# Kernel tuning notes

Measured on AMD Instinct MI355X. Metric: run time of the kernel, lower is better.

Reference implementation:

```python
import jax, jax.numpy as jnp
import numpy as np

K = 3  # polynomial filter order

def gfgcn_layer(X, S, W, h, b):
    # X: [N, in], W: [in, out], h: [K], b: [out]
    X = X @ W
    X_out = h[0] * X
    Sx = X
    for k in range(1, K):
        Sx = S @ Sx                 # graph shift propagation
        X_out = X_out + h[k] * Sx   # scalar-weighted accumulate
    return X_out + b[None, :]


def setup_inputs() -> dict:
    key = jax.random.key(0)
    ks = jax.random.split(key, 12)
    N, in_dim, hid_dim, out_dim = 8192, 512, 128, 64
    # scale S so repeated propagation stays numerically tame
    S = jax.random.normal(ks[0], (N, N), dtype=jnp.float32) / jnp.sqrt(jnp.float32(N))
    X = jax.random.normal(ks[1], (N, in_dim), dtype=jnp.float32)
    def kaiming(k, shape):
        bound = np.sqrt(6.0 / shape[0])
        return jax.random.uniform(k, shape, jnp.float32, -bound, bound)
    W1 = kaiming(ks[2], (in_dim, hid_dim))
    W2 = kaiming(ks[3], (hid_dim, hid_dim))
    W3 = kaiming(ks[4], (hid_dim, out_dim))
    h1 = jnp.ones((K,), jnp.float32)
    h2 = jnp.ones((K,), jnp.float32)
    h3 = jnp.ones((K,), jnp.float32)
    b1 = jnp.zeros((hid_dim,), jnp.float32)
    b2 = jnp.zeros((hid_dim,), jnp.float32)
    b3 = jnp.zeros((out_dim,), jnp.float32)
    return {"S": S, "X": X, "W1": W1, "h1": h1, "b1": b1,
            "W2": W2, "h2": h2, "b2": b2, "W3": W3, "h3": h3, "b3": b3}


def reference(S, X, W1, h1, b1, W2, h2, b2, W3, h3, b3):
    # layer 1 + ReLU (dropout p=0 -> identity, batch_norm=False)
    X = jax.nn.relu(gfgcn_layer(X, S, W1, h1, b1))
    # layer 2 + ReLU
    X = jax.nn.relu(gfgcn_layer(X, S, W2, h2, b2))
    # last layer, last_act = Identity
    return gfgcn_layer(X, S, W3, h3, b3)
```

## Files before the change

kernel.cpp:

```cpp
#include <hip/hip_runtime.h>


typedef __attribute__((ext_vector_type(4))) float  f32x4;
typedef __attribute__((ext_vector_type(8))) __bf16 bf16x8;
typedef __attribute__((ext_vector_type(4))) __bf16 bf16x4;

__device__ __forceinline__ void gload_lds16(const __bf16* g, __bf16* l) {
    __builtin_amdgcn_global_load_lds(
        (const __attribute__((address_space(1))) void*)g,
        (__attribute__((address_space(3))) void*)l, 16, 0, 0);
}

__global__ void cvt_f32_bf16(const float4* __restrict__ in,
                             bf16x4* __restrict__ out, int n4) {
    int i  = blockIdx.x * blockDim.x + threadIdx.x;
    int st = gridDim.x * blockDim.x;
    for (; i < n4; i += st) {
        float4 v = in[i];
        bf16x4 o;
        o[0] = (__bf16)v.x; o[1] = (__bf16)v.y;
        o[2] = (__bf16)v.z; o[3] = (__bf16)v.w;
        out[i] = o;
    }
}

__global__ void cvt_transpose(const float* __restrict__ W,
                              __bf16* __restrict__ Wt, int Kd, int Md) {
    int i = blockIdx.x * blockDim.x + threadIdx.x;
    if (i < Kd * Md) {
        int k = i / Md, m = i % Md;
        Wt[(size_t)m * Kd + k] = (__bf16)W[i];
    }
}

template<int MF, int NF, int OUTMODE>
__global__ __launch_bounds__(256)
void gemm_rd(const __bf16* __restrict__ A, const __bf16* __restrict__ Bt,
             void* __restrict__ out, int K, int Kchunk, int Mtot, int Ntot)
{
    const int lane = threadIdx.x & 63;
    const int w    = threadIdx.x >> 6;
    const int l15  = lane & 15;
    const int quad = lane >> 4;

    const int m_base = blockIdx.x * (64 * MF) + w * (16 * MF);
    const int n_base = blockIdx.y * (16 * NF);
    const int kstart = blockIdx.z * Kchunk;

    const __bf16* Ap[MF];
    #pragma unroll
    for (int mf = 0; mf < MF; mf++)
        Ap[mf] = A + (size_t)(m_base + mf * 16 + l15) * K + kstart + quad * 8;
    const __bf16* Bp[NF];
    #pragma unroll
    for (int nf = 0; nf < NF; nf++)
        Bp[nf] = Bt + (size_t)(n_base + nf * 16 + l15) * K + kstart + quad * 8;

    f32x4 acc[MF][NF];
    #pragma unroll
    for (int mf = 0; mf < MF; mf++)
        #pragma unroll
        for (int nf = 0; nf < NF; nf++)
            acc[mf][nf] = (f32x4){0.f, 0.f, 0.f, 0.f};

    #pragma unroll 2
    for (int ks = 0; ks < Kchunk; ks += 32) {
        bf16x8 a[MF], b[NF];
        #pragma unroll
        for (int mf = 0; mf < MF; mf++) a[mf] = *(const bf16x8*)(Ap[mf] + ks);
        #pragma unroll
        for (int nf = 0; nf < NF; nf++) b[nf] = *(const bf16x8*)(Bp[nf] + ks);
        #pragma unroll
        for (int mf = 0; mf < MF; mf++)
            #pragma unroll
            for (int nf = 0; nf < NF; nf++)
                acc[mf][nf] = __builtin_amdgcn_mfma_f32_16x16x32_bf16(
                    a[mf], b[nf], acc[mf][nf], 0, 0, 0);
    }

    if (OUTMODE == 0) {
        float* P = (float*)out + (size_t)blockIdx.z * Mtot * Ntot;
        #pragma unroll
        for (int mf = 0; mf < MF; mf++) {
            const int rowb = m_base + mf * 16 + quad * 4;
            #pragma unroll
            for (int nf = 0; nf < NF; nf++) {
                const int col = n_base + nf * 16 + l15;
                *(f32x4*)(P + (size_t)col * Mtot + rowb) = acc[mf][nf];
            }
        }
    } else {
        __bf16* O = (__bf16*)out;
        #pragma unroll
        for (int mf = 0; mf < MF; mf++) {
            const int rowb = m_base + mf * 16 + quad * 4;
            #pragma unroll
            for (int nf = 0; nf < NF; nf++) {
                const int col = n_base + nf * 16 + l15;
                #pragma unroll
                for (int r = 0; r < 4; r++)
                    O[(size_t)(rowb + r) * Ntot + col] = (__bf16)acc[mf][nf][r];
            }
        }
    }
}

template<int NFW>
__global__ __launch_bounds__(256)
void sgemm_lds(const __bf16* __restrict__ A, const __bf16* __restrict__ Bt,
               float* __restrict__ P, int K, int Kchunk, int Mtot)
{
    constexpr int BN = 32 * NFW;
    __shared__ __bf16 Asm[2][64 * 32];
    __shared__ __bf16 Bsm[2][BN * 32];

    const int t    = threadIdx.x;
    const int lane = t & 63;
    const int w    = t >> 6;
    const int wm   = w >> 1;
    const int wn   = w & 1;
    const int l15  = lane & 15;
    const int quad = lane >> 4;

    const int m_block = blockIdx.x * 64;
    const int kstart  = blockIdx.z * Kchunk;

    const int rt  = t >> 2;
    const int qs  = (t & 3) ^ ((rt >> 1) & 3);
    const __bf16* gA  = A  + (size_t)(m_block + rt) * K + kstart + qs * 8;
    const __bf16* gB0 = Bt + (size_t)rt * K        + kstart + qs * 8;
    const __bf16* gB1 = Bt + (size_t)(64 + rt) * K + kstart + qs * 8;

    f32x4 acc[2][NFW];
    #pragma unroll
    for (int mf = 0; mf < 2; mf++)
        #pragma unroll
        for (int nf = 0; nf < NFW; nf++)
            acc[mf][nf] = (f32x4){0.f, 0.f, 0.f, 0.f};

    auto stage = [&](int buf, int ks) {
        gload_lds16(gA  + ks, &Asm[buf][t * 8]);
        gload_lds16(gB0 + ks, &Bsm[buf][t * 8]);
        if (NFW == 4)
            gload_lds16(gB1 + ks, &Bsm[buf][2048 + t * 8]);
    };

    int aoff[2], boff[NFW];
    #pragma unroll
    for (int mf = 0; mf < 2; mf++) {
        const int ar = wm * 32 + mf * 16 + l15;
        aoff[mf] = ar * 32 + (quad ^ ((ar >> 1) & 3)) * 8;
    }
    #pragma unroll
    for (int nf = 0; nf < NFW; nf++) {
        const int br = wn * 16 * NFW + nf * 16 + l15;
        boff[nf] = br * 32 + (quad ^ ((br >> 1) & 3)) * 8;
    }

    stage(0, 0);
    __syncthreads();

    int buf = 0;
    for (int ks = 0; ; ) {
        const int nks = ks + 32;
        if (nks < Kchunk) stage(buf ^ 1, nks);

        bf16x8 a[2], b[NFW];
        #pragma unroll
        for (int mf = 0; mf < 2; mf++)
            a[mf] = *(const bf16x8*)&Asm[buf][aoff[mf]];
        #pragma unroll
        for (int nf = 0; nf < NFW; nf++)
            b[nf] = *(const bf16x8*)&Bsm[buf][boff[nf]];

        #pragma unroll
        for (int mf = 0; mf < 2; mf++)
            #pragma unroll
            for (int nf = 0; nf < NFW; nf++)
                acc[mf][nf] = __builtin_amdgcn_mfma_f32_16x16x32_bf16(
                    a[mf], b[nf], acc[mf][nf], 0, 0, 0);

        ks = nks;
        if (ks >= Kchunk) break;
        __syncthreads();
        buf ^= 1;
    }

    float* Pz = P + (size_t)blockIdx.z * Mtot * BN;
    #pragma unroll
    for (int mf = 0; mf < 2; mf++) {
        const int rowb = m_block + wm * 32 + mf * 16 + quad * 4;
        #pragma unroll
        for (int nf = 0; nf < NFW; nf++) {
            const int col = wn * 16 * NFW + nf * 16 + l15;
            *(f32x4*)(Pz + (size_t)col * Mtot + rowb) = acc[mf][nf];
        }
    }
}

__global__ void reduce_partials(const float* __restrict__ P,
                                __bf16* __restrict__ Y, int total4,
                                int SP, int MN) {
    int i = blockIdx.x * blockDim.x + threadIdx.x;
    if (i >= total4) return;
    size_t base = (size_t)i * 4;
    float4 s = *(const float4*)(P + base);
    for (int sp = 1; sp < SP; sp++) {
        float4 v = *(const float4*)(P + (size_t)sp * MN + base);
        s.x += v.x; s.y += v.y; s.z += v.z; s.w += v.w;
    }
    bf16x4 o; o[0] = (__bf16)s.x; o[1] = (__bf16)s.y;
    o[2] = (__bf16)s.z; o[3] = (__bf16)s.w;
    *(bf16x4*)(Y + base) = o;
}

template<int RELU, int F32OUT>
__global__ void combine_out(const float* __restrict__ P,
                            const __bf16* __restrict__ Y0t,
                            const __bf16* __restrict__ Y1t,
                            const float* __restrict__ h,
                            const float* __restrict__ bias,
                            void* __restrict__ outp,
                            int F, int SP) {
    const int i = blockIdx.x * blockDim.x + threadIdx.x;
    const int total = F * 2048;
    if (i >= total) return;
    const int f  = i >> 11;
    const int n4 = i & 2047;
    const size_t base = (size_t)f * 8192 + (size_t)n4 * 4;
    const int MN = F * 8192;

    float4 s = *(const float4*)(P + base);
    for (int sp = 1; sp < SP; sp++) {
        float4 v = *(const float4*)(P + (size_t)sp * MN + base);
        s.x += v.x; s.y += v.y; s.z += v.z; s.w += v.w;
    }
    bf16x4 y0 = *(const bf16x4*)(Y0t + base);
    bf16x4 y1 = *(const bf16x4*)(Y1t + base);
    const float h0 = h[0], h1 = h[1], h2 = h[2], bb = bias[f];

    float v[4] = {s.x, s.y, s.z, s.w};
    #pragma unroll
    for (int r = 0; r < 4; r++) {
        float x = h0 * (float)y0[r] + h1 * (float)y1[r] + h2 * v[r] + bb;
        if (RELU) x = fmaxf(x, 0.0f);
        v[r] = x;
    }
    const int node = n4 * 4;
    if (F32OUT) {
        float* O = (float*)outp;
        #pragma unroll
        for (int r = 0; r < 4; r++) O[(size_t)(node + r) * F + f] = v[r];
    } else {
        __bf16* O = (__bf16*)outp;
        #pragma unroll
        for (int r = 0; r < 4; r++) O[(size_t)(node + r) * F + f] = (__bf16)v[r];
    }
}

extern "C" void kernel_launch(void* const* d_in, const int* in_sizes, int n_in,
                              void* d_out, int out_size, void* d_ws, size_t ws_size,
                              hipStream_t stream) {
    const float* S  = (const float*)d_in[0];
    const float* X  = (const float*)d_in[1];
    const float* W1 = (const float*)d_in[2];
    const float* h1 = (const float*)d_in[3];
    const float* b1 = (const float*)d_in[4];
    const float* W2 = (const float*)d_in[5];
    const float* h2 = (const float*)d_in[6];
    const float* b2 = (const float*)d_in[7];
    const float* W3 = (const float*)d_in[8];
    const float* h3 = (const float*)d_in[9];
    const float* b3 = (const float*)d_in[10];
    float* out = (float*)d_out;

    const int Nn = 8192, IN = 512, HID = 128, OUT = 64;

    char* ws = (char*)d_ws;
    size_t off = 0;
    auto carve = [&](size_t bytes) -> void* {
        void* p = ws + off;
        off += (bytes + 255) & ~(size_t)255;
        return p;
    };
    __bf16* Sb  = (__bf16*)carve((size_t)Nn * Nn  * 2);
    __bf16* Xb  = (__bf16*)carve((size_t)Nn * IN  * 2);
    __bf16* W1t = (__bf16*)carve((size_t)IN  * HID * 2);
    __bf16* W2t = (__bf16*)carve((size_t)HID * HID * 2);
    __bf16* W3t = (__bf16*)carve((size_t)HID * OUT * 2);
    __bf16* Y0t = (__bf16*)carve((size_t)HID * Nn * 2);
    __bf16* Y1t = (__bf16*)carve((size_t)HID * Nn * 2);
    __bf16* Act = (__bf16*)carve((size_t)Nn * HID * 2);
    size_t  base = off;

    const size_t per_split = (size_t)HID * Nn * 4;
    int SP = 1;
    while (SP < 8 && base + (size_t)(SP * 2) * per_split <= ws_size) SP *= 2;
    float* P = (float*)carve((size_t)SP * per_split);
    const int KCH = Nn / SP;

    {
        int n4 = Nn * Nn / 4;
        cvt_f32_bf16<<<dim3((n4 + 255) / 256), dim3(256), 0, stream>>>(
            (const float4*)S, (bf16x4*)Sb, n4);
        n4 = Nn * IN / 4;
        cvt_f32_bf16<<<dim3((n4 + 255) / 256), dim3(256), 0, stream>>>(
            (const float4*)X, (bf16x4*)Xb, n4);
    }
    cvt_transpose<<<dim3((IN * HID + 255) / 256), dim3(256), 0, stream>>>(W1, W1t, IN, HID);
    cvt_transpose<<<dim3((HID * HID + 255) / 256), dim3(256), 0, stream>>>(W2, W2t, HID, HID);
    cvt_transpose<<<dim3((HID * OUT + 255) / 256), dim3(256), 0, stream>>>(W3, W3t, HID, OUT);

    auto sgemm = [&](const __bf16* Bt, int F) {
        if (F == 128)
            sgemm_lds<4><<<dim3(Nn / 64, 1, SP), dim3(256), 0, stream>>>(
                Sb, Bt, P, Nn, KCH, Nn);
        else
            sgemm_lds<2><<<dim3(Nn / 64, 1, SP), dim3(256), 0, stream>>>(
                Sb, Bt, P, Nn, KCH, Nn);
    };
    auto reduceY = [&](__bf16* Y, int F) {
        int t4 = F * 2048;
        reduce_partials<<<dim3((t4 + 255) / 256), dim3(256), 0, stream>>>(
            P, Y, t4, SP, F * Nn);
    };

    gemm_rd<2, 4, 1><<<dim3(1, Nn / 64, 1), dim3(256), 0, stream>>>(
        W1t, Xb, Y0t, IN, IN, HID, Nn);
    sgemm(Y0t, HID);
    reduceY(Y1t, HID);
    sgemm(Y1t, HID);
    combine_out<1, 0><<<dim3(HID * 2048 / 256), dim3(256), 0, stream>>>(
        P, Y0t, Y1t, h1, b1, Act, HID, SP);

    gemm_rd<2, 4, 1><<<dim3(1, Nn / 64, 1), dim3(256), 0, stream>>>(
        W2t, Act, Y0t, HID, HID, HID, Nn);
    sgemm(Y0t, HID);
    reduceY(Y1t, HID);
    sgemm(Y1t, HID);
    combine_out<1, 0><<<dim3(HID * 2048 / 256), dim3(256), 0, stream>>>(
        P, Y0t, Y1t, h2, b2, Act, HID, SP);

    gemm_rd<1, 4, 1><<<dim3(1, Nn / 64, 1), dim3(256), 0, stream>>>(
        W3t, Act, Y0t, HID, HID, OUT, Nn);
    sgemm(Y0t, OUT);
    reduceY(Y1t, OUT);
    sgemm(Y1t, OUT);
    combine_out<0, 1><<<dim3(OUT * 2048 / 256), dim3(256), 0, stream>>>(
        P, Y0t, Y1t, h3, b3, out, OUT, SP);

    (void)in_sizes; (void)n_in; (void)out_size;
}
```

Before: 710.4 us.

## Triple-buffer S-GEMM with vmcnt waits, fuse X conversion into first GEMM

The LDS-staged S-GEMM moves from a double buffer to a three-stage ring. It uses explicit s_waitcnt vmcnt counts and raw barriers so global-to-LDS loads run two stages ahead of the MFMA work. The separate X fp32-to-bf16 conversion kernel is removed, and the first dense GEMM now reads fp32 X directly and converts it in registers. The S conversion kernel switches to a fixed grid-stride launch. This adds more LDS use and a hand-tuned wait count that must match the number of outstanding loads, and the fused path reads twice the bytes of X per load.

```diff
diff --git a/kernel.cpp b/kernel.cpp
--- a/kernel.cpp
+++ b/kernel.cpp
@@ -33,9 +33,9 @@
     }
 }
 
-template<int MF, int NF, int OUTMODE>
+template<int MF, int NF, int OUTMODE, int BF32>
 __global__ __launch_bounds__(256)
-void gemm_rd(const __bf16* __restrict__ A, const __bf16* __restrict__ Bt,
+void gemm_rd(const __bf16* __restrict__ A, const void* __restrict__ Bv,
              void* __restrict__ out, int K, int Kchunk, int Mtot, int Ntot)
 {
     const int lane = threadIdx.x & 63;
@@ -51,10 +51,15 @@
     #pragma unroll
     for (int mf = 0; mf < MF; mf++)
         Ap[mf] = A + (size_t)(m_base + mf * 16 + l15) * K + kstart + quad * 8;
+
     const __bf16* Bp[NF];
-    #pragma unroll
-    for (int nf = 0; nf < NF; nf++)
-        Bp[nf] = Bt + (size_t)(n_base + nf * 16 + l15) * K + kstart + quad * 8;
+    const float*  Bpf[NF];
+    #pragma unroll
+    for (int nf = 0; nf < NF; nf++) {
+        const size_t roff = (size_t)(n_base + nf * 16 + l15) * K + kstart + quad * 8;
+        if (BF32) Bpf[nf] = (const float*)Bv + roff;
+        else      Bp[nf]  = (const __bf16*)Bv + roff;
+    }
 
     f32x4 acc[MF][NF];
     #pragma unroll
@@ -69,7 +74,20 @@
         #pragma unroll
         for (int mf = 0; mf < MF; mf++) a[mf] = *(const bf16x8*)(Ap[mf] + ks);
         #pragma unroll
-        for (int nf = 0; nf < NF; nf++) b[nf] = *(const bf16x8*)(Bp[nf] + ks);
+        for (int nf = 0; nf < NF; nf++) {
+            if (BF32) {
+                float4 f0 = *(const float4*)(Bpf[nf] + ks);
+                float4 f1 = *(const float4*)(Bpf[nf] + ks + 4);
+                bf16x8 tt;
+                tt[0] = (__bf16)f0.x; tt[1] = (__bf16)f0.y;
+                tt[2] = (__bf16)f0.z; tt[3] = (__bf16)f0.w;
+                tt[4] = (__bf16)f1.x; tt[5] = (__bf16)f1.y;
+                tt[6] = (__bf16)f1.z; tt[7] = (__bf16)f1.w;
+                b[nf] = tt;
+            } else {
+                b[nf] = *(const bf16x8*)(Bp[nf] + ks);
+            }
+        }
         #pragma unroll
         for (int mf = 0; mf < MF; mf++)
             #pragma unroll
@@ -111,8 +129,8 @@
                float* __restrict__ P, int K, int Kchunk, int Mtot)
 {
     constexpr int BN = 32 * NFW;
-    __shared__ __bf16 Asm[2][64 * 32];
-    __shared__ __bf16 Bsm[2][BN * 32];
+    __shared__ __bf16 Asm[3][64 * 32];
+    __shared__ __bf16 Bsm[3][BN * 32];
 
     const int t    = threadIdx.x;
     const int lane = t & 63;
@@ -124,6 +142,7 @@
 
     const int m_block = blockIdx.x * 64;
     const int kstart  = blockIdx.z * Kchunk;
+    const int nst     = Kchunk >> 5;
 
     const int rt  = t >> 2;
     const int qs  = (t & 3) ^ ((rt >> 1) & 3);
@@ -138,7 +157,8 @@
         for (int nf = 0; nf < NFW; nf++)
             acc[mf][nf] = (f32x4){0.f, 0.f, 0.f, 0.f};
 
-    auto stage = [&](int buf, int ks) {
+    auto stage = [&](int buf, int st) {
+        const int ks = st << 5;
         gload_lds16(gA  + ks, &Asm[buf][t * 8]);
         gload_lds16(gB0 + ks, &Bsm[buf][t * 8]);
         if (NFW == 4)
@@ -158,13 +178,26 @@
     }
 
     stage(0, 0);
-    __syncthreads();
-
-    int buf = 0;
-    for (int ks = 0; ; ) {
-        const int nks = ks + 32;
-        if (nks < Kchunk) stage(buf ^ 1, nks);
-
+    if (nst > 1) stage(1, 1);
+    if (nst > 2) stage(2, 2);
+
+    for (int st = 0; st < nst; ++st) {
+        const int rem   = nst - 1 - st;
+        const int ahead = rem < 2 ? rem : 2;
+
+        if (ahead == 2) {
+            if (NFW == 4) asm volatile("s_waitcnt vmcnt(6)" ::: "memory");
+            else          asm volatile("s_waitcnt vmcnt(4)" ::: "memory");
+        } else if (ahead == 1) {
+            if (NFW == 4) asm volatile("s_waitcnt vmcnt(3)" ::: "memory");
+            else          asm volatile("s_waitcnt vmcnt(2)" ::: "memory");
+        } else {
+            asm volatile("s_waitcnt vmcnt(0)" ::: "memory");
+        }
+        __builtin_amdgcn_s_barrier();
+        asm volatile("" ::: "memory");
+
+        const int buf = st - (st / 3) * 3;
         bf16x8 a[2], b[NFW];
         #pragma unroll
         for (int mf = 0; mf < 2; mf++)
@@ -172,6 +205,11 @@
         #pragma unroll
         for (int nf = 0; nf < NFW; nf++)
             b[nf] = *(const bf16x8*)&Bsm[buf][boff[nf]];
+
+        asm volatile("s_waitcnt lgkmcnt(0)" ::: "memory");
+        __builtin_amdgcn_s_barrier();
+        asm volatile("" ::: "memory");
+        if (st + 3 < nst) stage(buf, st + 3);
 
         #pragma unroll
         for (int mf = 0; mf < 2; mf++)
@@ -179,11 +217,6 @@
             for (int nf = 0; nf < NFW; nf++)
                 acc[mf][nf] = __builtin_amdgcn_mfma_f32_16x16x32_bf16(
                     a[mf], b[nf], acc[mf][nf], 0, 0, 0);
-
-        ks = nks;
-        if (ks >= Kchunk) break;
-        __syncthreads();
-        buf ^= 1;
     }
 
     float* Pz = P + (size_t)blockIdx.z * Mtot * BN;
@@ -284,7 +317,6 @@
         return p;
     };
     __bf16* Sb  = (__bf16*)carve((size_t)Nn * Nn  * 2);
-    __bf16* Xb  = (__bf16*)carve((size_t)Nn * IN  * 2);
     __bf16* W1t = (__bf16*)carve((size_t)IN  * HID * 2);
     __bf16* W2t = (__bf16*)carve((size_t)HID * HID * 2);
     __bf16* W3t = (__bf16*)carve((size_t)HID * OUT * 2);
@@ -301,11 +333,8 @@
 
     {
         int n4 = Nn * Nn / 4;
-        cvt_f32_bf16<<<dim3((n4 + 255) / 256), dim3(256), 0, stream>>>(
+        cvt_f32_bf16<<<dim3(4096), dim3(256), 0, stream>>>(
             (const float4*)S, (bf16x4*)Sb, n4);
-        n4 = Nn * IN / 4;
-        cvt_f32_bf16<<<dim3((n4 + 255) / 256), dim3(256), 0, stream>>>(
-            (const float4*)X, (bf16x4*)Xb, n4);
     }
     cvt_transpose<<<dim3((IN * HID + 255) / 256), dim3(256), 0, stream>>>(W1, W1t, IN, HID);
     cvt_transpose<<<dim3((HID * HID + 255) / 256), dim3(256), 0, stream>>>(W2, W2t, HID, HID);
@@ -325,15 +354,15 @@
             P, Y, t4, SP, F * Nn);
     };
 
-    gemm_rd<2, 4, 1><<<dim3(1, Nn / 64, 1), dim3(256), 0, stream>>>(
-        W1t, Xb, Y0t, IN, IN, HID, Nn);
+    gemm_rd<2, 4, 1, 1><<<dim3(1, Nn / 64, 1), dim3(256), 0, stream>>>(
+        W1t, X, Y0t, IN, IN, HID, Nn);
     sgemm(Y0t, HID);
     reduceY(Y1t, HID);
     sgemm(Y1t, HID);
     combine_out<1, 0><<<dim3(HID * 2048 / 256), dim3(256), 0, stream>>>(
         P, Y0t, Y1t, h1, b1, Act, HID, SP);
 
-    gemm_rd<2, 4, 1><<<dim3(1, Nn / 64, 1), dim3(256), 0, stream>>>(
+    gemm_rd<2, 4, 1, 0><<<dim3(1, Nn / 64, 1), dim3(256), 0, stream>>>(
         W2t, Act, Y0t, HID, HID, HID, Nn);
     sgemm(Y0t, HID);
     reduceY(Y1t, HID);
@@ -341,7 +370,7 @@
     combine_out<1, 0><<<dim3(HID * 2048 / 256), dim3(256), 0, stream>>>(
         P, Y0t, Y1t, h2, b2, Act, HID, SP);
 
-    gemm_rd<1, 4, 1><<<dim3(1, Nn / 64, 1), dim3(256), 0, stream>>>(
+    gemm_rd<1, 4, 1, 0><<<dim3(1, Nn / 64, 1), dim3(256), 0, stream>>>(
         W3t, Act, Y0t, HID, HID, OUT, Nn);
     sgemm(Y0t, OUT);
     reduceY(Y1t, OUT);
```

New measurement: 722.0 us. Within noise of the previous version (+1.6%).
